# Kernel tuning notes

Measured on AMD Instinct MI355X. Metric: run time of the kernel, lower is better.

Reference implementation:

```python
import jax, jax.numpy as jnp
import numpy as np

FFT_NORM = 'forward'


def setup_inputs() -> dict:
    key = jax.random.key(0)
    ks = jax.random.split(key, 6)
    B, N, Cin, Cout, T, M = 16, 16384, 64, 64, 256, 2049  # M = modes//2+1 with modes=4096
    x = jax.random.normal(ks[0], (B, N, Cin), dtype=jnp.float32)
    t_emb = jax.random.normal(ks[1], (B, T), dtype=jnp.float32)
    scale = 1.0 / jnp.sqrt(jnp.float32(Cin))
    weights_real = jax.random.normal(ks[2], (M, Cin, Cout), dtype=jnp.float32) * scale
    weights_imag = jax.random.normal(ks[3], (M, Cin, Cout), dtype=jnp.float32) * scale
    dense_real_w = jax.random.normal(ks[4], (M, T), dtype=jnp.float32) * (1.0 / jnp.sqrt(jnp.float32(T)))
    dense_imag_w = jax.random.normal(ks[5], (M, T), dtype=jnp.float32) * (1.0 / jnp.sqrt(jnp.float32(T)))
    return {"x": x, "t_emb": t_emb, "weights_real": weights_real,
            "weights_imag": weights_imag, "dense_real_w": dense_real_w,
            "dense_imag_w": dense_imag_w}


def reference(x, t_emb, weights_real, weights_imag, dense_real_w, dense_imag_w):
    B, N, _ = x.shape
    M, _, Cout = weights_real.shape  # M = modes//2+1
    W = weights_real + 1j * weights_imag  # (M, Cin, Cout) complex64
    # FFT along the grid axis
    x_ft = jnp.fft.rfft(x, axis=-2, norm=FFT_NORM)  # (B, N//2+1, Cin) complex64
    # Time modulation: eqx Linear (bias-free) = t_emb @ W^T
    t_mod = (t_emb @ dense_real_w.T) + 1j * (t_emb @ dense_imag_w.T)  # (B, M)
    # Diagonal modulation + channel mix, exactly equal to the eye/einsum pair:
    # out[b,i,o] = t_mod[b,i] * sum_c x_ft[b,i,c] * W[i,c,o]
    out_trunc = jnp.einsum('bi,bic,ico->bio', t_mod, x_ft[:, :M, :], W)  # (B, M, Cout)
    out_ft = jnp.zeros((B, N // 2 + 1, Cout), dtype=jnp.complex64)
    out_ft = out_ft.at[:, :M, :].set(out_trunc)
    out = jnp.fft.irfft(out_ft, axis=-2, n=N, norm=FFT_NORM)  # (B, N, Cout) float32
    return out
```

## Files before the change

### kernel.cpp

```cpp
#include <hip/hip_runtime.h>
#include <math.h>

#define B_   16
#define N_   16384
#define H_   8192
#define LOGH 13
#define CIN  64
#define COUT 64
#define T_   256
#define M_   2049

__device__ __forceinline__ unsigned br13(unsigned v) {
  return __brev(v) >> 19;
}

__device__ __forceinline__ int SW(int n) {
  return (n & ~31) | ((n ^ (n >> 5) ^ (n >> 10)) & 31);
}

__device__ __forceinline__ void cmul(float ar, float ai, float br, float bi,
                                     float& rr, float& ri) {
  rr = ar * br - ai * bi;
  ri = ar * bi + ai * br;
}

__device__ __constant__ float C16[16] = {
  1.f, 0.92387953251f, 0.70710678119f, 0.38268343236f, 0.f, -0.38268343236f,
  -0.70710678119f, -0.92387953251f, -1.f, -0.92387953251f, -0.70710678119f,
  -0.38268343236f, 0.f, 0.38268343236f, 0.70710678119f, 0.92387953251f};
__device__ __constant__ float S16[16] = {
  0.f, 0.38268343236f, 0.70710678119f, 0.92387953251f, 1.f, 0.92387953251f,
  0.70710678119f, 0.38268343236f, 0.f, -0.38268343236f, -0.70710678119f,
  -0.92387953251f, -1.f, -0.92387953251f, -0.70710678119f, -0.38268343236f};

template <int SIGN, int S0>
__device__ __forceinline__ void group16(float* __restrict__ sre,
                                        float* __restrict__ sim, int tid) {
  const int lo = tid & ((1 << S0) - 1);
  const int hi = tid >> S0;
  const int base = (hi << (S0 + 4)) + lo;
  int pp[16];
  float xr[16], xi[16];
#pragma unroll
  for (int j = 0; j < 16; ++j) {
    pp[j] = SW(base + (j << S0));
    xr[j] = sre[pp[j]];
    xi[j] = sim[pp[j]];
  }
  float th = 6.283185307179586f * (float)lo / (float)(16 << S0);
  float sn, cs;
  __sincosf(th, &sn, &cs);
  float w1r = cs, w1i = (float)SIGN * sn;
  float w2r, w2i, w4r, w4i, w8r, w8i;
  cmul(w1r, w1i, w1r, w1i, w2r, w2i);
  cmul(w2r, w2i, w2r, w2i, w4r, w4i);
  cmul(w4r, w4i, w4r, w4i, w8r, w8i);
  {
#pragma unroll
    for (int j = 0; j < 16; j += 2) {
      float br, bi;
      cmul(xr[j + 1], xi[j + 1], w8r, w8i, br, bi);
      xr[j + 1] = xr[j] - br; xi[j + 1] = xi[j] - bi;
      xr[j] += br; xi[j] += bi;
    }
  }
  {
    float tr[2], ti[2];
    tr[0] = w4r; ti[0] = w4i;
    cmul(w4r, w4i, C16[4], (float)SIGN * S16[4], tr[1], ti[1]);
#pragma unroll
    for (int j = 0; j < 16; ++j) {
      if ((j & 2) == 0) {
        int jl = j & 1;
        float br, bi;
        cmul(xr[j + 2], xi[j + 2], tr[jl], ti[jl], br, bi);
        xr[j + 2] = xr[j] - br; xi[j + 2] = xi[j] - bi;
        xr[j] += br; xi[j] += bi;
      }
    }
  }
  {
    float tr[4], ti[4];
#pragma unroll
    for (int jl = 0; jl < 4; ++jl)
      cmul(w2r, w2i, C16[2 * jl], (float)SIGN * S16[2 * jl], tr[jl], ti[jl]);
#pragma unroll
    for (int j = 0; j < 16; ++j) {
      if ((j & 4) == 0) {
        int jl = j & 3;
        float br, bi;
        cmul(xr[j + 4], xi[j + 4], tr[jl], ti[jl], br, bi);
        xr[j + 4] = xr[j] - br; xi[j + 4] = xi[j] - bi;
        xr[j] += br; xi[j] += bi;
      }
    }
  }
  {
    float tr[8], ti[8];
#pragma unroll
    for (int jl = 0; jl < 8; ++jl)
      cmul(w1r, w1i, C16[jl], (float)SIGN * S16[jl], tr[jl], ti[jl]);
#pragma unroll
    for (int j = 0; j < 8; ++j) {
      float br, bi;
      cmul(xr[j + 8], xi[j + 8], tr[j], ti[j], br, bi);
      xr[j + 8] = xr[j] - br; xi[j + 8] = xi[j] - bi;
      xr[j] += br; xi[j] += bi;
    }
  }
#pragma unroll
  for (int j = 0; j < 16; ++j) {
    sre[pp[j]] = xr[j];
    sim[pp[j]] = xi[j];
  }
}

template <int SIGN>
__device__ __forceinline__ void stageD(float* __restrict__ sre,
                                       float* __restrict__ sim, int tid) {
  float th = 6.283185307179586f * (float)tid / 8192.0f;
  float sn, cs;
  __sincosf(th, &sn, &cs);
  float wtr = cs, wti = (float)SIGN * sn;
#pragma unroll
  for (int s = 0; s < 8; ++s) {
    float twr, twi;
    cmul(wtr, wti, C16[s], (float)SIGN * S16[s], twr, twi);
    int i0 = tid + 512 * s;
    int p0 = SW(i0), p1 = SW(i0 + 4096);
    float br, bi;
    cmul(sre[p1], sim[p1], twr, twi, br, bi);
    float ar = sre[p0], ai = sim[p0];
    sre[p0] = ar + br; sim[p0] = ai + bi;
    sre[p1] = ar - br; sim[p1] = ai - bi;
  }
}

__global__ __launch_bounds__(256) void tmod_kernel(
    const float* __restrict__ t_emb,
    const float* __restrict__ dwr, const float* __restrict__ dwi,
    float* __restrict__ tmr, float* __restrict__ tmi) {
  int wave = threadIdx.x >> 6;
  int lane = threadIdx.x & 63;
  int p = blockIdx.x * 4 + wave;
  if (p >= B_ * M_) return;
  int b = p / M_, i = p % M_;
  float ar = 0.f, ai = 0.f;
  for (int j = 0; j < 4; ++j) {
    int t = lane + 64 * j;
    float te = t_emb[b * T_ + t];
    ar += te * dwr[(size_t)i * T_ + t];
    ai += te * dwi[(size_t)i * T_ + t];
  }
  for (int off = 32; off > 0; off >>= 1) {
    ar += __shfl_down(ar, off, 64);
    ai += __shfl_down(ai, off, 64);
  }
  if (lane == 0) { tmr[b * M_ + i] = ar; tmi[b * M_ + i] = ai; }
}

__global__ __launch_bounds__(256) void pack_transpose(
    const float* __restrict__ x, float* __restrict__ zre, float* __restrict__ zim) {
  __shared__ float tile[64][65];
  int b = blockIdx.y, nt = blockIdx.x;
  int n0 = nt * 64;
  int j  = threadIdx.x & 63;
  int iy = threadIdx.x >> 6;
  for (int p = 0; p < 16; ++p) {
    int i = iy + 4 * p;
    tile[i][j] = x[((size_t)(b * N_ + n0 + i)) * CIN + j];
  }
  __syncthreads();
  int ii = threadIdx.x & 31;
  int cy = threadIdx.x >> 5;
  int h0 = nt * 32;
  for (int p = 0; p < 8; ++p) {
    int c = cy + 8 * p;
    size_t o = (size_t)(b * CIN + c) * H_ + h0 + ii;
    zre[o] = tile[2 * ii][c];
    zim[o] = tile[2 * ii + 1][c];
  }
}

__global__ __launch_bounds__(512, 4) void fft_fwd(
    const float* __restrict__ zre, const float* __restrict__ zim,
    float* __restrict__ Xre, float* __restrict__ Xim) {
  __shared__ float sre[H_], sim[H_];
  int bc = blockIdx.x;
  int tid = threadIdx.x;
  size_t base = (size_t)bc * H_;
#pragma unroll
  for (int s = 0; s < 16; ++s) {
    int n = tid + 512 * s;
    int r = SW((int)br13(n));
    sre[r] = zre[base + n];
    sim[r] = zim[base + n];
  }
  __syncthreads();
  group16<-1, 0>(sre, sim, tid); __syncthreads();
  group16<-1, 4>(sre, sim, tid); __syncthreads();
  group16<-1, 8>(sre, sim, tid); __syncthreads();
  stageD<-1>(sre, sim, tid);     __syncthreads();
  const float sc = 1.0f / (float)N_;
  for (int k = tid; k < M_; k += 512) {
    int mk = (H_ - k) & (H_ - 1);
    int pk = SW(k), pm = SW(mk);
    float zr = sre[pk], zi = sim[pk];
    float mr = sre[pm], mi = -sim[pm];
    float Er = 0.5f * (zr + mr), Ei = 0.5f * (zi + mi);
    float Dr = zr - mr,          Di = zi - mi;
    float Or = 0.5f * Di,        Oi = -0.5f * Dr;
    float ang = -6.283185307179586f * (float)k / (float)N_;
    float sn, cs;
    __sincosf(ang, &sn, &cs);
    float Xr = Er + cs * Or - sn * Oi;
    float Xi = Ei + cs * Oi + sn * Or;
    Xre[(size_t)bc * M_ + k] = Xr * sc;
    Xim[(size_t)bc * M_ + k] = Xi * sc;
  }
}

__global__ __launch_bounds__(256) void transpose2(
    const float* __restrict__ s0, const float* __restrict__ s1,
    float* __restrict__ d0, float* __restrict__ d1, int R, int C) {
  __shared__ float tile[32][33];
  const float* src = blockIdx.z ? s1 : s0;
  float* dst = blockIdx.z ? d1 : d0;
  int c0 = blockIdx.x * 32, r0 = blockIdx.y * 32;
  int tx = threadIdx.x & 31, ty = threadIdx.x >> 5;
  for (int p = 0; p < 32; p += 8) {
    int r = r0 + ty + p, c = c0 + tx;
    tile[ty + p][tx] = (r < R && c < C) ? src[(size_t)r * C + c] : 0.f;
  }
  __syncthreads();
  for (int p = 0; p < 32; p += 8) {
    int r = c0 + ty + p, c = r0 + tx;
    if (r < C && c < R) dst[(size_t)r * R + c] = tile[tx][ty + p];
  }
}

typedef short  s8v  __attribute__((ext_vector_type(8)));
typedef float  f4v  __attribute__((ext_vector_type(4)));

__device__ __forceinline__ unsigned short f2bf_hi(float x) {
  unsigned u = __float_as_uint(x);
  unsigned r = (u + 0x7fffu + ((u >> 16) & 1u)) >> 16;
  return (unsigned short)r;
}

__device__ __forceinline__ int fbi(int k, int n) {
  return ((((n >> 4) * 2 + (k >> 5)) << 9) | (((n & 15) + (((k >> 3) & 3) << 4)) << 3) | (k & 7));
}
__device__ __forceinline__ int fai(int k, int m) {
  return (((k >> 5) << 9) | (((m & 15) + (((k >> 3) & 3) << 4)) << 3) | (k & 7));
}

__global__ __launch_bounds__(256) void mix_mfma(
    const float* __restrict__ Xtr, const float* __restrict__ Xti,
    const float* __restrict__ Wr_g, const float* __restrict__ Wi_g,
    const float* __restrict__ tmr, const float* __restrict__ tmi,
    float* __restrict__ Yr_g, float* __restrict__ Yi_g) {
  __shared__ __align__(16) unsigned short BrH[4096], BrL[4096], BiH[4096], BiL[4096];
  __shared__ __align__(16) unsigned short ArH[1024], ArL[1024];
  __shared__ __align__(16) unsigned short AiH[1024], AiL[1024];
  __shared__ __align__(16) unsigned short AnH[1024], AnL[1024];
  __shared__ float tms[32];
  const int i   = blockIdx.x;
  const int tid = threadIdx.x;

  const float4* wr4 = (const float4*)(Wr_g + (size_t)i * 4096);
  const float4* wi4 = (const float4*)(Wi_g + (size_t)i * 4096);
#pragma unroll
  for (int it = 0; it < 4; ++it) {
    int f4 = it * 256 + tid;
    float4 vr = wr4[f4];
    float4 vi = wi4[f4];
    int idx0 = f4 * 4;
    float er[4] = {vr.x, vr.y, vr.z, vr.w};
    float ei[4] = {vi.x, vi.y, vi.z, vi.w};
#pragma unroll
    for (int e = 0; e < 4; ++e) {
      int idx = idx0 + e;
      int k = idx >> 6, n = idx & 63;
      int a = fbi(k, n);
      unsigned short h = f2bf_hi(er[e]);
      float hf = __uint_as_float(((unsigned)h) << 16);
      BrH[a] = h; BrL[a] = f2bf_hi(er[e] - hf);
      h = f2bf_hi(ei[e]);
      hf = __uint_as_float(((unsigned)h) << 16);
      BiH[a] = h; BiL[a] = f2bf_hi(ei[e] - hf);
    }
  }
  {
    float4 vr = ((const float4*)(Xtr + (size_t)i * 1024))[tid];
    float4 vi = ((const float4*)(Xti + (size_t)i * 1024))[tid];
    float er[4] = {vr.x, vr.y, vr.z, vr.w};
    float ei[4] = {vi.x, vi.y, vi.z, vi.w};
    int idx0 = tid * 4;
#pragma unroll
    for (int e = 0; e < 4; ++e) {
      int idx = idx0 + e;
      int m = idx >> 6, k = idx & 63;
      int a = fai(k, m);
      unsigned short h = f2bf_hi(er[e]);
      float hf = __uint_as_float(((unsigned)h) << 16);
      ArH[a] = h; ArL[a] = f2bf_hi(er[e] - hf);
      h = f2bf_hi(ei[e]);
      hf = __uint_as_float(((unsigned)h) << 16);
      unsigned short l = f2bf_hi(ei[e] - __uint_as_float(((unsigned)h) << 16));
      AiH[a] = h; AiL[a] = l;
      AnH[a] = h ^ 0x8000u; AnL[a] = l ^ 0x8000u;
    }
  }
  if (tid < 16) {
    tms[tid]      = tmr[tid * M_ + i];
    tms[16 + tid] = tmi[tid * M_ + i];
  }
  __syncthreads();

  const int w = tid >> 6, L = tid & 63;
  const s8v* pArH = (const s8v*)ArH; const s8v* pArL = (const s8v*)ArL;
  const s8v* pAiH = (const s8v*)AiH; const s8v* pAiL = (const s8v*)AiL;
  const s8v* pAnH = (const s8v*)AnH; const s8v* pAnL = (const s8v*)AnL;
  const s8v* pBrH = (const s8v*)BrH; const s8v* pBrL = (const s8v*)BrL;
  const s8v* pBiH = (const s8v*)BiH; const s8v* pBiL = (const s8v*)BiL;

  f4v cr = {0.f, 0.f, 0.f, 0.f}, ci = {0.f, 0.f, 0.f, 0.f};
#pragma unroll
  for (int s = 0; s < 2; ++s) {
    s8v arh = pArH[s * 64 + L], arl = pArL[s * 64 + L];
    s8v aih = pAiH[s * 64 + L], ail = pAiL[s * 64 + L];
    s8v anh = pAnH[s * 64 + L], anl = pAnL[s * 64 + L];
    int bo = (w * 2 + s) * 64 + L;
    s8v brh = pBrH[bo], brl = pBrL[bo];
    s8v bih = pBiH[bo], bil = pBiL[bo];
    cr = __builtin_amdgcn_mfma_f32_16x16x32_bf16(arh, brh, cr, 0, 0, 0);
    cr = __builtin_amdgcn_mfma_f32_16x16x32_bf16(arh, brl, cr, 0, 0, 0);
    cr = __builtin_amdgcn_mfma_f32_16x16x32_bf16(arl, brh, cr, 0, 0, 0);
    cr = __builtin_amdgcn_mfma_f32_16x16x32_bf16(anh, bih, cr, 0, 0, 0);
    cr = __builtin_amdgcn_mfma_f32_16x16x32_bf16(anh, bil, cr, 0, 0, 0);
    cr = __builtin_amdgcn_mfma_f32_16x16x32_bf16(anl, bih, cr, 0, 0, 0);
    ci = __builtin_amdgcn_mfma_f32_16x16x32_bf16(arh, bih, ci, 0, 0, 0);
    ci = __builtin_amdgcn_mfma_f32_16x16x32_bf16(arh, bil, ci, 0, 0, 0);
    ci = __builtin_amdgcn_mfma_f32_16x16x32_bf16(arl, bih, ci, 0, 0, 0);
    ci = __builtin_amdgcn_mfma_f32_16x16x32_bf16(aih, brh, ci, 0, 0, 0);
    ci = __builtin_amdgcn_mfma_f32_16x16x32_bf16(aih, brl, ci, 0, 0, 0);
    ci = __builtin_amdgcn_mfma_f32_16x16x32_bf16(ail, brh, ci, 0, 0, 0);
  }

  const int n = (L & 15) + 16 * w;
  const int quad = L >> 4;
#pragma unroll
  for (int r = 0; r < 4; ++r) {
    int m = quad * 4 + r;
    float tr = tms[m], ti = tms[16 + m];
    float yr = tr * cr[r] - ti * ci[r];
    float yi = tr * ci[r] + ti * cr[r];
    size_t o = (size_t)i * 1024 + m * 64 + n;
    Yr_g[o] = yr;
    Yi_g[o] = yi;
  }
}

__global__ __launch_bounds__(512, 4) void fft_inv(
    const float* __restrict__ Ytr, const float* __restrict__ Yti,
    float* __restrict__ zre, float* __restrict__ zim) {
  __shared__ float sre[H_], sim[H_];
  int bo = blockIdx.x;
  int tid = threadIdx.x;
  size_t ybase = (size_t)bo * M_;
#pragma unroll
  for (int s = 0; s < 16; ++s) {
    int k = tid + 512 * s;
    float ykr = 0.f, yki = 0.f, ymr = 0.f, ymi = 0.f;
    if (k < M_) { ykr = Ytr[ybase + k]; yki = Yti[ybase + k]; }
    int m = H_ - k;
    if (m < M_) { ymr = Ytr[ybase + m]; ymi = -Yti[ybase + m]; }
    float Sr = ykr + ymr, Si = yki + ymi;
    float Dr = ykr - ymr, Di = yki - ymi;
    float ang = 6.283185307179586f * (float)k / (float)N_;
    float sn, cs;
    __sincosf(ang, &sn, &cs);
    float Zr = Sr - (cs * Di + sn * Dr);
    float Zi = Si + (cs * Dr - sn * Di);
    int r = SW((int)br13(k));
    sre[r] = Zr; sim[r] = Zi;
  }
  __syncthreads();
  group16<1, 0>(sre, sim, tid); __syncthreads();
  group16<1, 4>(sre, sim, tid); __syncthreads();
  group16<1, 8>(sre, sim, tid); __syncthreads();
  stageD<1>(sre, sim, tid);     __syncthreads();
  size_t base = (size_t)bo * H_;
#pragma unroll
  for (int s = 0; s < 16; ++s) {
    int n = tid + 512 * s;
    int p = SW(n);
    zre[base + n] = sre[p];
    zim[base + n] = sim[p];
  }
}

__global__ __launch_bounds__(256) void unpack_transpose(
    const float* __restrict__ zre, const float* __restrict__ zim,
    float* __restrict__ out) {
  __shared__ float tre[64][33], tim[64][33];
  int b = blockIdx.y, ht = blockIdx.x;
  int h0 = ht * 32;
  int ii = threadIdx.x & 31, cy = threadIdx.x >> 5;
  for (int p = 0; p < 8; ++p) {
    int c = cy + 8 * p;
    size_t idx = (size_t)(b * COUT + c) * H_ + h0 + ii;
    tre[c][ii] = zre[idx];
    tim[c][ii] = zim[idx];
  }
  __syncthreads();
  int o = threadIdx.x & 63, ry = threadIdx.x >> 6;
  for (int p = 0; p < 16; ++p) {
    int r = ry + 4 * p;
    int n = h0 * 2 + r;
    float v = (r & 1) ? tim[o][r >> 1] : tre[o][r >> 1];
    out[((size_t)(b * N_ + n)) * COUT + o] = v;
  }
}

extern "C" void kernel_launch(void* const* d_in, const int* in_sizes, int n_in,
                              void* d_out, int out_size, void* d_ws, size_t ws_size,
                              hipStream_t stream) {
  const float* x    = (const float*)d_in[0];
  const float* temb = (const float*)d_in[1];
  const float* wr   = (const float*)d_in[2];
  const float* wi   = (const float*)d_in[3];
  const float* dwr  = (const float*)d_in[4];
  const float* dwi  = (const float*)d_in[5];
  float* out = (float*)d_out;

  float* ws  = (float*)d_ws;
  float* tmr = ws;
  float* tmi = tmr + 32784;
  float* zre = tmi + 32784;
  float* zim = zre + 8388608;
  float* Xre = zim + 8388608;
  float* Xim = Xre + 2098176;
  float* Xtr = Xim + 2098176;
  float* Xti = Xtr + 2098176;

  tmod_kernel<<<dim3((B_ * M_ + 3) / 4), 256, 0, stream>>>(temb, dwr, dwi, tmr, tmi);
  pack_transpose<<<dim3(N_ / 64, B_), 256, 0, stream>>>(x, zre, zim);
  fft_fwd<<<dim3(B_ * CIN), 512, 0, stream>>>(zre, zim, Xre, Xim);
  transpose2<<<dim3((M_ + 31) / 32, (B_ * CIN + 31) / 32, 2), 256, 0, stream>>>(
      Xre, Xim, Xtr, Xti, B_ * CIN, M_);
  mix_mfma<<<dim3(M_), 256, 0, stream>>>(Xtr, Xti, wr, wi, tmr, tmi, Xtr, Xti);
  transpose2<<<dim3((B_ * COUT + 31) / 32, (M_ + 31) / 32, 2), 256, 0, stream>>>(
      Xtr, Xti, Xre, Xim, M_, B_ * COUT);
  fft_inv<<<dim3(B_ * COUT), 512, 0, stream>>>(Xre, Xim, zre, zim);
  unpack_transpose<<<dim3(H_ / 32, B_), 256, 0, stream>>>(zre, zim, out);
}
```

Before: 286.8 us.

## Fuse transposes into FFT and mix kernels with XCD-aware block remapping

Removes the two separate transpose kernels. The forward FFT now writes its output directly in mode-major layout, and the channel-mix kernel writes its output directly in the (b,o)-major layout that the inverse FFT reads. Block indices are remapped in both kernels, apparently so that blocks on the same XCD touch nearby columns and writes coalesce better in L2. The trade-off is that the writes become strided or scattered instead of contiguous. The mix grid is padded to 2056 blocks, with early exits for the extra ones.

```diff
diff --git a/kernel.cpp b/kernel.cpp
--- a/kernel.cpp
+++ b/kernel.cpp
@@ -184,9 +184,10 @@
 
 __global__ __launch_bounds__(512, 4) void fft_fwd(
     const float* __restrict__ zre, const float* __restrict__ zim,
-    float* __restrict__ Xre, float* __restrict__ Xim) {
+    float* __restrict__ Xtr, float* __restrict__ Xti) {
   __shared__ float sre[H_], sim[H_];
-  int bc = blockIdx.x;
+  int hw = blockIdx.x;
+  int bc = ((hw & 7) << 7) | (hw >> 3);
   int tid = threadIdx.x;
   size_t base = (size_t)bc * H_;
 #pragma unroll
@@ -215,27 +216,8 @@
     __sincosf(ang, &sn, &cs);
     float Xr = Er + cs * Or - sn * Oi;
     float Xi = Ei + cs * Oi + sn * Or;
-    Xre[(size_t)bc * M_ + k] = Xr * sc;
-    Xim[(size_t)bc * M_ + k] = Xi * sc;
-  }
-}
-
-__global__ __launch_bounds__(256) void transpose2(
-    const float* __restrict__ s0, const float* __restrict__ s1,
-    float* __restrict__ d0, float* __restrict__ d1, int R, int C) {
-  __shared__ float tile[32][33];
-  const float* src = blockIdx.z ? s1 : s0;
-  float* dst = blockIdx.z ? d1 : d0;
-  int c0 = blockIdx.x * 32, r0 = blockIdx.y * 32;
-  int tx = threadIdx.x & 31, ty = threadIdx.x >> 5;
-  for (int p = 0; p < 32; p += 8) {
-    int r = r0 + ty + p, c = c0 + tx;
-    tile[ty + p][tx] = (r < R && c < C) ? src[(size_t)r * C + c] : 0.f;
-  }
-  __syncthreads();
-  for (int p = 0; p < 32; p += 8) {
-    int r = c0 + ty + p, c = r0 + tx;
-    if (r < C && c < R) dst[(size_t)r * R + c] = tile[tx][ty + p];
+    Xtr[(size_t)k * 1024 + bc] = Xr * sc;
+    Xti[(size_t)k * 1024 + bc] = Xi * sc;
   }
 }
 
@@ -259,13 +241,15 @@
     const float* __restrict__ Xtr, const float* __restrict__ Xti,
     const float* __restrict__ Wr_g, const float* __restrict__ Wi_g,
     const float* __restrict__ tmr, const float* __restrict__ tmi,
-    float* __restrict__ Yr_g, float* __restrict__ Yi_g) {
+    float* __restrict__ Ytr, float* __restrict__ Yti) {
   __shared__ __align__(16) unsigned short BrH[4096], BrL[4096], BiH[4096], BiL[4096];
   __shared__ __align__(16) unsigned short ArH[1024], ArL[1024];
   __shared__ __align__(16) unsigned short AiH[1024], AiL[1024];
   __shared__ __align__(16) unsigned short AnH[1024], AnL[1024];
   __shared__ float tms[32];
-  const int i   = blockIdx.x;
+  const int hw = blockIdx.x;
+  const int i  = (hw & 7) * 257 + (hw >> 3);
+  if ((hw >> 3) >= 257 || i >= M_) return;
   const int tid = threadIdx.x;
 
   const float4* wr4 = (const float4*)(Wr_g + (size_t)i * 4096);
@@ -356,9 +340,9 @@
     float tr = tms[m], ti = tms[16 + m];
     float yr = tr * cr[r] - ti * ci[r];
     float yi = tr * ci[r] + ti * cr[r];
-    size_t o = (size_t)i * 1024 + m * 64 + n;
-    Yr_g[o] = yr;
-    Yi_g[o] = yi;
+    size_t o = (size_t)(m * 64 + n) * M_ + i;
+    Ytr[o] = yr;
+    Yti[o] = yi;
   }
 }
 
@@ -440,19 +424,15 @@
   float* tmi = tmr + 32784;
   float* zre = tmi + 32784;
   float* zim = zre + 8388608;
-  float* Xre = zim + 8388608;
-  float* Xim = Xre + 2098176;
-  float* Xtr = Xim + 2098176;
+  float* Xtr = zim + 8388608;
   float* Xti = Xtr + 2098176;
+  float* Ytr = Xti + 2098176;
+  float* Yti = Ytr + 2098176;
 
   tmod_kernel<<<dim3((B_ * M_ + 3) / 4), 256, 0, stream>>>(temb, dwr, dwi, tmr, tmi);
   pack_transpose<<<dim3(N_ / 64, B_), 256, 0, stream>>>(x, zre, zim);
-  fft_fwd<<<dim3(B_ * CIN), 512, 0, stream>>>(zre, zim, Xre, Xim);
-  transpose2<<<dim3((M_ + 31) / 32, (B_ * CIN + 31) / 32, 2), 256, 0, stream>>>(
-      Xre, Xim, Xtr, Xti, B_ * CIN, M_);
-  mix_mfma<<<dim3(M_), 256, 0, stream>>>(Xtr, Xti, wr, wi, tmr, tmi, Xtr, Xti);
-  transpose2<<<dim3((B_ * COUT + 31) / 32, (M_ + 31) / 32, 2), 256, 0, stream>>>(
-      Xtr, Xti, Xre, Xim, M_, B_ * COUT);
-  fft_inv<<<dim3(B_ * COUT), 512, 0, stream>>>(Xre, Xim, zre, zim);
+  fft_fwd<<<dim3(B_ * CIN), 512, 0, stream>>>(zre, zim, Xtr, Xti);
+  mix_mfma<<<dim3(2056), 256, 0, stream>>>(Xtr, Xti, wr, wi, tmr, tmi, Ytr, Yti);
+  fft_inv<<<dim3(B_ * COUT), 512, 0, stream>>>(Ytr, Yti, zre, zim);
   unpack_transpose<<<dim3(H_ / 32, B_), 256, 0, stream>>>(zre, zim, out);
 }
```

Result: slower. 304.9 us (+6.3%).
